# Kernel tuning notes

Measured on AMD Instinct MI355X. Metric: run time of the kernel, lower is better.

The kernel has to match this reference:

```python
import jax, jax.numpy as jnp
import numpy as np

N = 100_000           # nodes
E = 3_200_000         # edges (avg degree 32)
DIMS = [64, 80, 160, 112, 160, 176, 96, 144, 96, 128, 96, 160]
NUM_CLASSES = 2


def setup_inputs() -> dict:
    key = jax.random.key(0)
    ks = jax.random.split(key, 64)
    inp = {}
    inp['x'] = jax.random.normal(ks[0], (N, DIMS[0]), dtype=jnp.float32)
    inp['src'] = jax.random.randint(ks[1], (E,), 0, N, dtype=jnp.int32)
    inp['dst'] = jax.random.randint(ks[2], (E,), 0, N, dtype=jnp.int32)
    inp['edata'] = jax.random.uniform(ks[3], (E,), dtype=jnp.float32)
    for i in range(11):
        fi, fo = DIMS[i], DIMS[i + 1]
        inp[f'W{i+1}'] = jax.random.normal(ks[4 + i], (fi, fo), dtype=jnp.float32) / np.float32(np.sqrt(fi))
        inp[f'b{i+1}'] = jnp.zeros((fo,), dtype=jnp.float32)
    inp['Wd1'] = jax.random.normal(ks[20], (160, 140), dtype=jnp.float32) / np.float32(np.sqrt(160))
    inp['bd1'] = jnp.zeros((140,), dtype=jnp.float32)
    inp['Wd2'] = jax.random.normal(ks[21], (140, NUM_CLASSES), dtype=jnp.float32) / np.float32(np.sqrt(140))
    inp['bd2'] = jnp.zeros((NUM_CLASSES,), dtype=jnp.float32)
    inp['mu'] = jnp.asarray(0.0, dtype=jnp.float32)
    inp['sigma'] = jnp.asarray(1.0, dtype=jnp.float32)
    return inp


def _forward(x, src, dst, edata, Ws, bs, Wd1, bd1, Wd2, bd2, mu, sigma):
    n = x.shape[0]
    # edge-weight transform: keep w=1 edges, else gaussian kernel; mu/sigma read via .item() -> stop_gradient
    mu_c = jax.lax.stop_gradient(mu)
    sg_c = jax.lax.stop_gradient(sigma)
    w = jnp.where(edata == 1.0, edata, jnp.exp(-((edata - mu_c) ** 2) / sg_c))  # [E]
    ones_e = jnp.ones_like(edata)
    deg_out = jax.ops.segment_sum(ones_e, src, num_segments=n)  # [N]
    deg_in = jax.ops.segment_sum(ones_e, dst, num_segments=n)   # [N]
    ns = jnp.where(deg_out > 0, jax.lax.rsqrt(jnp.maximum(deg_out, 1.0)), 0.0)
    nd = jnp.where(deg_in > 0, jax.lax.rsqrt(jnp.maximum(deg_in, 1.0)), 0.0)
    coef = ns[src] * w  # [E] src-side norm fused with edge weight

    h = x
    for W, b in zip(Ws, bs):
        m = h[src] * coef[:, None]                               # gather + weight  [E, F]
        agg = jax.ops.segment_sum(m, dst, num_segments=n)        # scatter-add      [N, F]
        h = jax.nn.leaky_relu((agg * nd[:, None]) @ W + b)       # norm + linear + act

    h = jax.nn.leaky_relu(jnp.mean(h, axis=0))                   # mean_nodes -> [160]
    h = jax.nn.leaky_relu(h @ Wd1 + bd1)                         # dropout = identity (eval)
    return jax.nn.sigmoid(h @ Wd2 + bd2)                         # [NUM_CLASSES]


def reference(x, src, dst, edata,
              W1, b1, W2, b2, W3, b3, W4, b4, W5, b5, W6, b6,
              W7, b7, W8, b8, W9, b9, W10, b10, W11, b11,
              Wd1, bd1, Wd2, bd2, mu, sigma):
    Ws = [W1, W2, W3, W4, W5, W6, W7, W8, W9, W10, W11]
    bs = [b1, b2, b3, b4, b5, b6, b7, b8, b9, b10, b11]
    return _forward(x, src, dst, edata, Ws, bs, Wd1, bd1, Wd2, bd2, mu, sigma)
```

## Files before the change

### kernel.cpp

```cpp
#include <hip/hip_runtime.h>

#define LEAKY(v) ((v) > 0.0f ? (v) : 0.01f * (v))
#define SCAN_BLK 1024
#define EPB 4096
#define BKN 256

typedef __bf16 bf16x8 __attribute__((ext_vector_type(8)));
typedef float f32x4 __attribute__((ext_vector_type(4)));

__device__ inline float bflo(unsigned int u) { return __uint_as_float(u << 16); }
__device__ inline float bfhi(unsigned int u) { return __uint_as_float(u & 0xFFFF0000u); }
__device__ inline unsigned int pack2bf(float lo, float hi) {
    unsigned int a = __float_as_uint(lo);
    unsigned int b = __float_as_uint(hi);
    a = (a + 0x7FFFu + ((a >> 16) & 1u)) >> 16;
    b = (b + 0x7FFFu + ((b >> 16) & 1u)) & 0xFFFF0000u;
    return a | b;
}
__device__ inline unsigned short f2bf(float f) {
    unsigned int u = __float_as_uint(f);
    return (unsigned short)((u + 0x7FFFu + ((u >> 16) & 1u)) >> 16);
}

__device__ inline unsigned char f2f8(float v) {
    return (unsigned char)(__builtin_amdgcn_cvt_pk_fp8_f32(v, 0.0f, 0u, false) & 0xFFu);
}
__device__ inline uint2 pack8f8(float v0, float v1, float v2, float v3,
                                float v4, float v5, float v6, float v7) {
    uint2 q;
    q.x = __builtin_amdgcn_cvt_pk_fp8_f32(v0, v1, 0u, false);
    q.x = __builtin_amdgcn_cvt_pk_fp8_f32(v2, v3, q.x, true);
    q.y = __builtin_amdgcn_cvt_pk_fp8_f32(v4, v5, 0u, false);
    q.y = __builtin_amdgcn_cvt_pk_fp8_f32(v6, v7, q.y, true);
    return q;
}


__global__ void histo_kernel(const int* __restrict__ src, const int* __restrict__ dst,
                             int* __restrict__ bh_src, int* __restrict__ bh_dst,
                             int E, int NBK, int NBLK) {
    extern __shared__ int lds[];
    int* hs = lds;
    int* hd = lds + NBK;
    for (int j = threadIdx.x; j < 2 * NBK; j += 256) lds[j] = 0;
    __syncthreads();
    int b = blockIdx.x;
    int e0 = b * EPB, e1 = min(e0 + EPB, E);
    for (int e = e0 + threadIdx.x; e < e1; e += 256) {
        atomicAdd(&hs[src[e] >> 8], 1);
        atomicAdd(&hd[dst[e] >> 8], 1);
    }
    __syncthreads();
    for (int j = threadIdx.x; j < NBK; j += 256) {
        bh_src[j * NBLK + b] = hs[j];
        bh_dst[j * NBLK + b] = hd[j];
    }
}

__global__ void scan1_kernel(const int* __restrict__ deg, int* __restrict__ out,
                             int* __restrict__ bsums, int n) {
    __shared__ int sh[SCAN_BLK];
    int gid = blockIdx.x * SCAN_BLK + threadIdx.x;
    int v = (gid < n) ? deg[gid] : 0;
    sh[threadIdx.x] = v;
    __syncthreads();
    for (int off = 1; off < SCAN_BLK; off <<= 1) {
        int t = (threadIdx.x >= off) ? sh[threadIdx.x - off] : 0;
        __syncthreads();
        sh[threadIdx.x] += t;
        __syncthreads();
    }
    if (gid < n) out[gid + 1] = sh[threadIdx.x];
    if (threadIdx.x == SCAN_BLK - 1) bsums[blockIdx.x] = sh[threadIdx.x];
    if (gid == 0) out[0] = 0;
}

__global__ void scan2_kernel(int* __restrict__ bsums, int nb) {
    __shared__ int sh[SCAN_BLK];
    int v = (threadIdx.x < nb) ? bsums[threadIdx.x] : 0;
    sh[threadIdx.x] = v;
    __syncthreads();
    for (int off = 1; off < SCAN_BLK; off <<= 1) {
        int t = (threadIdx.x >= off) ? sh[threadIdx.x - off] : 0;
        __syncthreads();
        sh[threadIdx.x] += t;
        __syncthreads();
    }
    if (threadIdx.x < nb) bsums[threadIdx.x] = sh[threadIdx.x] - v;
}

__global__ void scan3_kernel(int* __restrict__ out, const int* __restrict__ bsums, int n) {
    int gid = blockIdx.x * SCAN_BLK + threadIdx.x;
    if (gid < n) out[gid + 1] += bsums[blockIdx.x];
}

__global__ void scat_src_kernel(const int* __restrict__ src, const int* __restrict__ bhs_src,
                                int* __restrict__ srcb, int E, int NBK, int NBLK) {
    extern __shared__ int cur[];
    int b = blockIdx.x;
    for (int j = threadIdx.x; j < NBK; j += 256) cur[j] = bhs_src[j * NBLK + b];
    __syncthreads();
    int e0 = b * EPB, e1 = min(e0 + EPB, E);
    for (int e = e0 + threadIdx.x; e < e1; e += 256) {
        int s = src[e];
        int pos = atomicAdd(&cur[s >> 8], 1);
        srcb[pos] = s;
    }
}

__global__ void ns_kernel(const int* __restrict__ srcb, const int* __restrict__ bhs_src,
                          float* __restrict__ ns, int n, int NBLK) {
    __shared__ int cnt[BKN];
    int b = blockIdx.x;
    int j = threadIdx.x;
    cnt[j] = 0;
    __syncthreads();
    int base = bhs_src[b * NBLK];
    int endp = bhs_src[(b + 1) * NBLK];
    for (int e = base + j; e < endp; e += 256)
        atomicAdd(&cnt[srcb[e] & 255], 1);
    __syncthreads();
    int node = b * BKN + j;
    if (node < n) {
        int c = cnt[j];
        ns[node] = (c > 0) ? rsqrtf((float)c) : 0.0f;
    }
}

__global__ void scat_dst_kernel(const int* __restrict__ src, const int* __restrict__ dst,
                                const float* __restrict__ edata, const float* __restrict__ ns,
                                const float* __restrict__ mu, const float* __restrict__ sigma,
                                const int* __restrict__ bhs_dst, int2* __restrict__ pay,
                                float* __restrict__ payw, int E, int NBK, int NBLK) {
    extern __shared__ int cur[];
    int b = blockIdx.x;
    for (int j = threadIdx.x; j < NBK; j += 256) cur[j] = bhs_dst[j * NBLK + b];
    __syncthreads();
    int e0 = b * EPB, e1 = min(e0 + EPB, E);
    for (int e = e0 + threadIdx.x; e < e1; e += 256) {
        int d = dst[e];
        int s = src[e];
        float ed = edata[e];
        float dd = ed - mu[0];
        float w = (ed == 1.0f) ? ed : expf(-(dd * dd) / sigma[0]);
        int pos = atomicAdd(&cur[d >> 8], 1);
        pay[pos] = make_int2(d, s);
        payw[pos] = ns[s] * w;
    }
}

__global__ void csr_kernel(const int2* __restrict__ pay, const float* __restrict__ payw,
                           const int* __restrict__ bhs_dst, int* __restrict__ rowptr,
                           float* __restrict__ nd, int2* __restrict__ es,
                           int n, int E, int NBK, int NBLK) {
    __shared__ int cnt[BKN];
    __shared__ int cur[BKN];
    int b = blockIdx.x;
    int j = threadIdx.x;
    cnt[j] = 0;
    __syncthreads();
    int base = bhs_dst[b * NBLK];
    int endp = bhs_dst[(b + 1) * NBLK];
    for (int e = base + j; e < endp; e += 256)
        atomicAdd(&cnt[pay[e].x & 255], 1);
    __syncthreads();
    int c0 = cnt[j];
    for (int off = 1; off < 256; off <<= 1) {
        int t = (j >= off) ? cnt[j - off] : 0;
        __syncthreads();
        cnt[j] += t;
        __syncthreads();
    }
    int excl = cnt[j] - c0;
    cur[j] = base + excl;
    int node = b * BKN + j;
    if (node < n) {
        rowptr[node] = base + excl;
        nd[node] = (c0 > 0) ? rsqrtf((float)c0) : 0.0f;
    }
    if (b == NBK - 1 && j == 0) rowptr[n] = E;
    __syncthreads();
    for (int e = base + j; e < endp; e += 256) {
        int2 p = pay[e];
        int pos = atomicAdd(&cur[p.x & 255], 1);
        es[pos] = make_int2(p.y, __float_as_int(payw[e]));
    }
}


__global__ void x2bf_kernel(const float* __restrict__ x, unsigned short* __restrict__ o16,
                            unsigned char* __restrict__ o8, long long total4) {
    long long i = (long long)blockIdx.x * blockDim.x + threadIdx.x;
    if (i < total4) {
        float4 v = *reinterpret_cast<const float4*>(&x[i * 4]);
        uint2 p;
        p.x = pack2bf(v.x, v.y);
        p.y = pack2bf(v.z, v.w);
        *reinterpret_cast<uint2*>(&o16[i * 4]) = p;
        unsigned int q = __builtin_amdgcn_cvt_pk_fp8_f32(v.x, v.y, 0u, false);
        q = __builtin_amdgcn_cvt_pk_fp8_f32(v.z, v.w, q, true);
        *reinterpret_cast<unsigned int*>(&o8[i * 4]) = q;
    }
}

__global__ void packW_kernel(const float* __restrict__ W, unsigned short* __restrict__ Wp,
                             int FI, int FO) {
    int KB = (FI + 31) / 32;
    int NB = FO / 16;
    int gid = blockIdx.x * blockDim.x + threadIdx.x;
    if (gid >= KB * NB * 64) return;
    int l = gid & 63;
    int tile = gid >> 6;
    int kb = tile % KB;
    int nb = tile / KB;
    int n = nb * 16 + (l & 15);
    int k0 = kb * 32 + (l >> 4) * 8;
    unsigned short tmp[8];
    #pragma unroll
    for (int j = 0; j < 8; ++j) {
        int k = k0 + j;
        tmp[j] = (k < FI) ? f2bf(W[(size_t)k * FO + n]) : (unsigned short)0;
    }
    *reinterpret_cast<uint4*>(&Wp[(size_t)gid * 8]) = *reinterpret_cast<uint4*>(tmp);
}

#define F8ACC(v, cc) { \
    auto p01 = __builtin_amdgcn_cvt_pk_f32_fp8((v).x, false); \
    auto p23 = __builtin_amdgcn_cvt_pk_f32_fp8((v).x, true);  \
    auto p45 = __builtin_amdgcn_cvt_pk_f32_fp8((v).y, false); \
    auto p67 = __builtin_amdgcn_cvt_pk_f32_fp8((v).y, true);  \
    a0 = fmaf(p01[0], cc, a0); a1 = fmaf(p01[1], cc, a1); \
    a2 = fmaf(p23[0], cc, a2); a3 = fmaf(p23[1], cc, a3); \
    a4 = fmaf(p45[0], cc, a4); a5 = fmaf(p45[1], cc, a5); \
    a6 = fmaf(p67[0], cc, a6); a7 = fmaf(p67[1], cc, a7); }

template<int MODE>
__global__ void agg_kernel(const unsigned char* __restrict__ h8,
                           const int* __restrict__ rowptr, const int2* __restrict__ es,
                           const float* __restrict__ nd, const float* __restrict__ bias,
                           unsigned short* __restrict__ out16, unsigned char* __restrict__ out8,
                           int n, int jt, int ng) {
    int g = threadIdx.x / jt;
    if (g >= ng) return;
    int i = blockIdx.x * ng + g;
    if (i >= n) return;
    int c = (threadIdx.x - g * jt) << 3;
    int F = jt << 3;
    int beg = rowptr[i], end = rowptr[i + 1];
    float a0 = 0, a1 = 0, a2 = 0, a3 = 0, a4 = 0, a5 = 0, a6 = 0, a7 = 0;
    int e = beg;
    for (; e + 4 <= end; e += 4) {
        int2 e0 = es[e + 0], e1 = es[e + 1], e2 = es[e + 2], e3 = es[e + 3];
        uint2 v0 = *reinterpret_cast<const uint2*>(&h8[(size_t)e0.x * F + c]);
        uint2 v1 = *reinterpret_cast<const uint2*>(&h8[(size_t)e1.x * F + c]);
        uint2 v2 = *reinterpret_cast<const uint2*>(&h8[(size_t)e2.x * F + c]);
        uint2 v3 = *reinterpret_cast<const uint2*>(&h8[(size_t)e3.x * F + c]);
        float c0 = __int_as_float(e0.y), c1 = __int_as_float(e1.y);
        float c2 = __int_as_float(e2.y), c3 = __int_as_float(e3.y);
        F8ACC(v0, c0)
        F8ACC(v1, c1)
        F8ACC(v2, c2)
        F8ACC(v3, c3)
    }
    for (; e < end; ++e) {
        int2 e0 = es[e];
        uint2 v0 = *reinterpret_cast<const uint2*>(&h8[(size_t)e0.x * F + c]);
        float c0 = __int_as_float(e0.y);
        F8ACC(v0, c0)
    }
    if (MODE) {
        float s = nd[i];
        a0 = a0 * s + bias[c + 0]; a0 = LEAKY(a0);
        a1 = a1 * s + bias[c + 1]; a1 = LEAKY(a1);
        a2 = a2 * s + bias[c + 2]; a2 = LEAKY(a2);
        a3 = a3 * s + bias[c + 3]; a3 = LEAKY(a3);
        a4 = a4 * s + bias[c + 4]; a4 = LEAKY(a4);
        a5 = a5 * s + bias[c + 5]; a5 = LEAKY(a5);
        a6 = a6 * s + bias[c + 6]; a6 = LEAKY(a6);
        a7 = a7 * s + bias[c + 7]; a7 = LEAKY(a7);
    }
    uint4 p;
    p.x = pack2bf(a0, a1); p.y = pack2bf(a2, a3);
    p.z = pack2bf(a4, a5); p.w = pack2bf(a6, a7);
    *reinterpret_cast<uint4*>(&out16[(size_t)i * F + c]) = p;
    if (MODE) {
        uint2 q = pack8f8(a0, a1, a2, a3, a4, a5, a6, a7);
        *reinterpret_cast<uint2*>(&out8[(size_t)i * F + c]) = q;
    }
}

template<int FI, int FO, int MODE>
__global__ __launch_bounds__(256) void mm_mfma_kernel(
    const unsigned short* __restrict__ Ab, const float* __restrict__ nd,
    const unsigned short* __restrict__ Wp, const float* __restrict__ bias,
    unsigned short* __restrict__ out16, unsigned char* __restrict__ out8, int n)
{
    constexpr int FIP = (FI + 31) / 32 * 32;
    constexpr int KB = FIP / 32;
    constexpr int NB = FO / 16;
    constexpr int LDA = FIP + 8;
    constexpr int RW = FIP / 8;
    __shared__ unsigned short As[64 * LDA];

    const int t = threadIdx.x;
    const int row0 = blockIdx.x * 64;

    for (int idx = t; idx < 64 * RW; idx += 256) {
        int r = idx / RW;
        int c8 = (idx - r * RW) * 8;
        int grow = row0 + r;
        uint4 v = make_uint4(0u, 0u, 0u, 0u);
        if (grow < n && c8 < FI)
            v = *reinterpret_cast<const uint4*>(&Ab[(size_t)grow * FI + c8]);
        *reinterpret_cast<uint4*>(&As[r * LDA + c8]) = v;
    }
    __syncthreads();

    const int w = t >> 6;
    const int l = t & 63;
    const int arow = (w << 4) + (l & 15);
    const int koff = (l >> 4) << 3;

    bf16x8 a[KB];
    #pragma unroll
    for (int kb = 0; kb < KB; ++kb)
        a[kb] = *reinterpret_cast<const bf16x8*>(&As[arow * LDA + kb * 32 + koff]);

    f32x4 acc[NB] = {};
    #pragma unroll
    for (int nb = 0; nb < NB; ++nb) {
        #pragma unroll
        for (int kb = 0; kb < KB; ++kb) {
            bf16x8 b = *reinterpret_cast<const bf16x8*>(&Wp[(size_t)((nb * KB + kb) * 64 + l) * 8]);
            acc[nb] = __builtin_amdgcn_mfma_f32_16x16x32_bf16(a[kb], b, acc[nb], 0, 0, 0);
        }
    }

    const int col = l & 15;
    const int rb = (l >> 4) << 2;
    #pragma unroll
    for (int r = 0; r < 4; ++r) {
        int grow = row0 + (w << 4) + rb + r;
        if (grow < n) {
            float s = MODE ? nd[grow] : 1.0f;
            #pragma unroll
            for (int nb = 0; nb < NB; ++nb) {
                float v = acc[nb][r];
                if (MODE) {
                    v = v * s + bias[nb * 16 + col];
                    v = LEAKY(v);
                    out16[(size_t)grow * FO + nb * 16 + col] = f2bf(v);
                    out8[(size_t)grow * FO + nb * 16 + col] = f2f8(v);
                } else {
                    out8[(size_t)grow * FO + nb * 16 + col] = f2f8(v);
                }
            }
        }
    }
}

__global__ void mean_kernel(const unsigned short* __restrict__ h, float* __restrict__ acc,
                            int n, int F) {
    int f = threadIdx.x;
    if (f >= F) return;
    float partial = 0.0f;
    for (int i = blockIdx.x; i < n; i += gridDim.x) {
        partial += __uint_as_float(((unsigned int)h[(size_t)i * F + f]) << 16);
    }
    atomicAdd(&acc[f], partial);
}

__global__ void head_kernel(const float* __restrict__ acc, const float* __restrict__ Wd1,
                            const float* __restrict__ bd1, const float* __restrict__ Wd2,
                            const float* __restrict__ bd2, float* __restrict__ out, int n) {
    __shared__ float gm[160];
    __shared__ float h1[140];
    int tid = threadIdx.x;
    if (tid < 160) {
        float v = acc[tid] / (float)n;
        gm[tid] = LEAKY(v);
    }
    __syncthreads();
    if (tid < 140) {
        float s = bd1[tid];
        for (int k = 0; k < 160; ++k) s += gm[k] * Wd1[k * 140 + tid];
        h1[tid] = LEAKY(s);
    }
    __syncthreads();
    if (tid < 2) {
        float s = bd2[tid];
        for (int k = 0; k < 140; ++k) s += h1[k] * Wd2[k * 2 + tid];
        out[tid] = 1.0f / (1.0f + expf(-s));
    }
}

extern "C" void kernel_launch(void* const* d_in, const int* in_sizes, int n_in,
                              void* d_out, int out_size, void* d_ws, size_t ws_size,
                              hipStream_t stream) {
    static const int dims[12] = {64, 80, 160, 112, 160, 176, 96, 144, 96, 128, 96, 160};

    const float* x     = (const float*)d_in[0];
    const int*   src   = (const int*)d_in[1];
    const int*   dst   = (const int*)d_in[2];
    const float* edata = (const float*)d_in[3];
    const float* W[11];
    const float* B[11];
    for (int i = 0; i < 11; ++i) {
        W[i] = (const float*)d_in[4 + 2 * i];
        B[i] = (const float*)d_in[5 + 2 * i];
    }
    const float* Wd1   = (const float*)d_in[26];
    const float* bd1   = (const float*)d_in[27];
    const float* Wd2   = (const float*)d_in[28];
    const float* bd2   = (const float*)d_in[29];
    const float* mu    = (const float*)d_in[30];
    const float* sigma = (const float*)d_in[31];
    float* out = (float*)d_out;

    const int N = in_sizes[0] / 64;
    const int E = in_sizes[1];
    const int FMAX = 176;

    const int NBK  = (N + BKN - 1) / BKN;
    const int NBLK = (E + EPB - 1) / EPB;
    const int LEN  = NBK * NBLK;

    size_t woff[11];
    size_t wtot = 0;
    for (int l = 0; l < 11; ++l) {
        woff[l] = wtot;
        int fip = (dims[l] + 31) / 32 * 32;
        wtot += (size_t)fip * dims[l + 1];
    }

    char* wsb = (char*)d_ws;
    size_t o = 0;
    auto alloc = [&](size_t bytes) { void* p = wsb + o; o += (bytes + 255) & ~(size_t)255; return p; };
    unsigned short* hb_main = (unsigned short*)alloc((size_t)N * FMAX * 2);
    unsigned short* hb_t    = (unsigned short*)alloc((size_t)N * FMAX * 2);
    unsigned char*  h8_main = (unsigned char*) alloc((size_t)N * FMAX);
    unsigned char*  h8_t    = (unsigned char*) alloc((size_t)N * FMAX);
    unsigned short* Wp  = (unsigned short*)alloc(wtot * 2);
    int2*  es      = (int2*) alloc((size_t)E * sizeof(int2));
    int2*  pay     = (int2*) alloc((size_t)E * sizeof(int2));
    float* payw    = (float*)alloc((size_t)E * sizeof(float));
    int*   srcb    = (int*)  alloc((size_t)E * sizeof(int));
    int*   bh_src  = (int*)  alloc((size_t)LEN * sizeof(int));
    int*   bhs_src = (int*)  alloc((size_t)(LEN + 1) * sizeof(int));
    int*   bh_dst  = (int*)  alloc((size_t)LEN * sizeof(int));
    int*   bhs_dst = (int*)  alloc((size_t)(LEN + 1) * sizeof(int));
    int*   rowptr  = (int*)  alloc((size_t)(N + 1) * sizeof(int));
    float* ns      = (float*)alloc((size_t)N * sizeof(float));
    float* nd      = (float*)alloc((size_t)N * sizeof(float));
    int*   bsums   = (int*)  alloc(2048 * sizeof(int));
    float* acc     = (float*)alloc(160 * sizeof(float));

    histo_kernel<<<NBLK, 256, 2 * NBK * sizeof(int), stream>>>(src, dst, bh_src, bh_dst,
                                                               E, NBK, NBLK);
    int snb = (LEN + SCAN_BLK - 1) / SCAN_BLK;
    scan1_kernel<<<snb, SCAN_BLK, 0, stream>>>(bh_src, bhs_src, bsums, LEN);
    scan2_kernel<<<1, SCAN_BLK, 0, stream>>>(bsums, snb);
    scan3_kernel<<<snb, SCAN_BLK, 0, stream>>>(bhs_src, bsums, LEN);
    scan1_kernel<<<snb, SCAN_BLK, 0, stream>>>(bh_dst, bhs_dst, bsums, LEN);
    scan2_kernel<<<1, SCAN_BLK, 0, stream>>>(bsums, snb);
    scan3_kernel<<<snb, SCAN_BLK, 0, stream>>>(bhs_dst, bsums, LEN);
    scat_src_kernel<<<NBLK, 256, NBK * sizeof(int), stream>>>(src, bhs_src, srcb, E, NBK, NBLK);
    ns_kernel<<<NBK, 256, 0, stream>>>(srcb, bhs_src, ns, N, NBLK);
    scat_dst_kernel<<<NBLK, 256, NBK * sizeof(int), stream>>>(src, dst, edata, ns, mu, sigma,
                                                              bhs_dst, pay, payw, E, NBK, NBLK);
    csr_kernel<<<NBK, 256, 0, stream>>>(pay, payw, bhs_dst, rowptr, nd, es, N, E, NBK, NBLK);

    long long x4 = (long long)N * 64 / 4;
    x2bf_kernel<<<(int)((x4 + 255) / 256), 256, 0, stream>>>(x, hb_main, h8_main, x4);
    for (int l = 0; l < 11; ++l) {
        int fip = (dims[l] + 31) / 32 * 32;
        int threads = (fip / 32) * (dims[l + 1] / 16) * 64;
        packW_kernel<<<(threads + 255) / 256, 256, 0, stream>>>(W[l], Wp + woff[l],
                                                                dims[l], dims[l + 1]);
    }

    const int mmgrid = (N + 63) / 64;

    #define DO_A(FI, FO, l) { \
        constexpr int jt = FI / 8; constexpr int ng = 256 / jt; \
        agg_kernel<0><<<(N + ng - 1) / ng, 256, 0, stream>>>( \
            h8_main, rowptr, es, nd, B[l], hb_t, nullptr, N, jt, ng); \
        mm_mfma_kernel<FI, FO, 1><<<mmgrid, 256, 0, stream>>>( \
            hb_t, nd, Wp + woff[l], B[l], hb_main, h8_main, N); }

    #define DO_B(FI, FO, l) { \
        mm_mfma_kernel<FI, FO, 0><<<mmgrid, 256, 0, stream>>>( \
            hb_main, nd, Wp + woff[l], B[l], nullptr, h8_t, N); \
        constexpr int jt = FO / 8; constexpr int ng = 256 / jt; \
        agg_kernel<1><<<(N + ng - 1) / ng, 256, 0, stream>>>( \
            h8_t, rowptr, es, nd, B[l], hb_main, h8_main, N, jt, ng); }

    DO_A(64, 80, 0)
    DO_A(80, 160, 1)
    DO_B(160, 112, 2)
    DO_A(112, 160, 3)
    DO_A(160, 176, 4)
    DO_B(176, 96, 5)
    DO_A(96, 144, 6)
    DO_B(144, 96, 7)
    DO_A(96, 128, 8)
    DO_B(128, 96, 9)
    DO_A(96, 160, 10)

    #undef DO_A
    #undef DO_B

    hipMemsetAsync(acc, 0, 160 * sizeof(float), stream);
    mean_kernel<<<256, 160, 0, stream>>>(hb_main, acc, N, 160);
    head_kernel<<<1, 256, 0, stream>>>(acc, Wd1, bd1, Wd2, bd2, out, N);
}
```

Before: 1.379 ms.

## Fuse src/dst bucket scatter, merge histogram scans, compact payloads, unroll aggregation by 8

Concatenates the src and dst bucket histograms so a single three-kernel scan covers both, and fuses the two scatter passes into one kernel with 512 threads. The payload is compacted: only the low 8 bits of each src id are stored for the degree count, and the dst low byte is packed into the top byte of the src id. The ns multiplication moves into the CSR build, so scatter no longer depends on ns. The aggregation inner loop is unrolled to eight edges to expose more memory-level parallelism, at the cost of more registers. Packing src into 24 bits assumes fewer than 16M nodes.

New measurement: 1.349 ms. -2.2%, faster.

```diff
diff --git a/kernel.cpp b/kernel.cpp
--- a/kernel.cpp
+++ b/kernel.cpp
@@ -37,23 +37,22 @@
 
 
 __global__ void histo_kernel(const int* __restrict__ src, const int* __restrict__ dst,
-                             int* __restrict__ bh_src, int* __restrict__ bh_dst,
-                             int E, int NBK, int NBLK) {
+                             int* __restrict__ bh, int E, int NBK, int NBLK, int LEN) {
     extern __shared__ int lds[];
     int* hs = lds;
     int* hd = lds + NBK;
-    for (int j = threadIdx.x; j < 2 * NBK; j += 256) lds[j] = 0;
+    for (int j = threadIdx.x; j < 2 * NBK; j += 512) lds[j] = 0;
     __syncthreads();
     int b = blockIdx.x;
     int e0 = b * EPB, e1 = min(e0 + EPB, E);
-    for (int e = e0 + threadIdx.x; e < e1; e += 256) {
+    for (int e = e0 + threadIdx.x; e < e1; e += 512) {
         atomicAdd(&hs[src[e] >> 8], 1);
         atomicAdd(&hd[dst[e] >> 8], 1);
     }
     __syncthreads();
-    for (int j = threadIdx.x; j < NBK; j += 256) {
-        bh_src[j * NBLK + b] = hs[j];
-        bh_dst[j * NBLK + b] = hd[j];
+    for (int j = threadIdx.x; j < NBK; j += 512) {
+        bh[j * NBLK + b] = hs[j];
+        bh[LEN + j * NBLK + b] = hd[j];
     }
 }
 
@@ -94,31 +93,45 @@
     if (gid < n) out[gid + 1] += bsums[blockIdx.x];
 }
 
-__global__ void scat_src_kernel(const int* __restrict__ src, const int* __restrict__ bhs_src,
-                                int* __restrict__ srcb, int E, int NBK, int NBLK) {
+__global__ void scat_kernel(const int* __restrict__ src, const int* __restrict__ dst,
+                            const float* __restrict__ edata,
+                            const float* __restrict__ mu, const float* __restrict__ sigma,
+                            const int* __restrict__ bhs, unsigned char* __restrict__ srcb8,
+                            int2* __restrict__ pay, int E, int NBK, int NBLK, int LEN) {
     extern __shared__ int cur[];
+    int* cs = cur;
+    int* cd = cur + NBK;
     int b = blockIdx.x;
-    for (int j = threadIdx.x; j < NBK; j += 256) cur[j] = bhs_src[j * NBLK + b];
+    for (int j = threadIdx.x; j < NBK; j += 512) {
+        cs[j] = bhs[j * NBLK + b];
+        cd[j] = bhs[LEN + j * NBLK + b] - E;
+    }
     __syncthreads();
     int e0 = b * EPB, e1 = min(e0 + EPB, E);
-    for (int e = e0 + threadIdx.x; e < e1; e += 256) {
+    for (int e = e0 + threadIdx.x; e < e1; e += 512) {
         int s = src[e];
-        int pos = atomicAdd(&cur[s >> 8], 1);
-        srcb[pos] = s;
-    }
-}
-
-__global__ void ns_kernel(const int* __restrict__ srcb, const int* __restrict__ bhs_src,
+        int d = dst[e];
+        float ed = edata[e];
+        float dd = ed - mu[0];
+        float w = (ed == 1.0f) ? ed : expf(-(dd * dd) / sigma[0]);
+        int ps = atomicAdd(&cs[s >> 8], 1);
+        srcb8[ps] = (unsigned char)(s & 255);
+        int pd = atomicAdd(&cd[d >> 8], 1);
+        pay[pd] = make_int2(s | ((d & 255) << 24), __float_as_int(w));
+    }
+}
+
+__global__ void ns_kernel(const unsigned char* __restrict__ srcb8, const int* __restrict__ bhs,
                           float* __restrict__ ns, int n, int NBLK) {
     __shared__ int cnt[BKN];
     int b = blockIdx.x;
     int j = threadIdx.x;
     cnt[j] = 0;
     __syncthreads();
-    int base = bhs_src[b * NBLK];
-    int endp = bhs_src[(b + 1) * NBLK];
+    int base = bhs[b * NBLK];
+    int endp = bhs[(b + 1) * NBLK];
     for (int e = base + j; e < endp; e += 256)
-        atomicAdd(&cnt[srcb[e] & 255], 1);
+        atomicAdd(&cnt[srcb8[e]], 1);
     __syncthreads();
     int node = b * BKN + j;
     if (node < n) {
@@ -127,42 +140,20 @@
     }
 }
 
-__global__ void scat_dst_kernel(const int* __restrict__ src, const int* __restrict__ dst,
-                                const float* __restrict__ edata, const float* __restrict__ ns,
-                                const float* __restrict__ mu, const float* __restrict__ sigma,
-                                const int* __restrict__ bhs_dst, int2* __restrict__ pay,
-                                float* __restrict__ payw, int E, int NBK, int NBLK) {
-    extern __shared__ int cur[];
-    int b = blockIdx.x;
-    for (int j = threadIdx.x; j < NBK; j += 256) cur[j] = bhs_dst[j * NBLK + b];
-    __syncthreads();
-    int e0 = b * EPB, e1 = min(e0 + EPB, E);
-    for (int e = e0 + threadIdx.x; e < e1; e += 256) {
-        int d = dst[e];
-        int s = src[e];
-        float ed = edata[e];
-        float dd = ed - mu[0];
-        float w = (ed == 1.0f) ? ed : expf(-(dd * dd) / sigma[0]);
-        int pos = atomicAdd(&cur[d >> 8], 1);
-        pay[pos] = make_int2(d, s);
-        payw[pos] = ns[s] * w;
-    }
-}
-
-__global__ void csr_kernel(const int2* __restrict__ pay, const float* __restrict__ payw,
-                           const int* __restrict__ bhs_dst, int* __restrict__ rowptr,
+__global__ void csr_kernel(const int2* __restrict__ pay, const float* __restrict__ ns,
+                           const int* __restrict__ bhs, int* __restrict__ rowptr,
                            float* __restrict__ nd, int2* __restrict__ es,
-                           int n, int E, int NBK, int NBLK) {
+                           int n, int E, int NBK, int NBLK, int LEN) {
     __shared__ int cnt[BKN];
     __shared__ int cur[BKN];
     int b = blockIdx.x;
     int j = threadIdx.x;
     cnt[j] = 0;
     __syncthreads();
-    int base = bhs_dst[b * NBLK];
-    int endp = bhs_dst[(b + 1) * NBLK];
+    int base = bhs[LEN + b * NBLK] - E;
+    int endp = bhs[LEN + (b + 1) * NBLK] - E;
     for (int e = base + j; e < endp; e += 256)
-        atomicAdd(&cnt[pay[e].x & 255], 1);
+        atomicAdd(&cnt[(pay[e].x >> 24) & 255], 1);
     __syncthreads();
     int c0 = cnt[j];
     for (int off = 1; off < 256; off <<= 1) {
@@ -182,8 +173,10 @@
     __syncthreads();
     for (int e = base + j; e < endp; e += 256) {
         int2 p = pay[e];
-        int pos = atomicAdd(&cur[p.x & 255], 1);
-        es[pos] = make_int2(p.y, __float_as_int(payw[e]));
+        int s = p.x & 0x00FFFFFF;
+        float coef = ns[s] * __int_as_float(p.y);
+        int pos = atomicAdd(&cur[(p.x >> 24) & 255], 1);
+        es[pos] = make_int2(s, __float_as_int(coef));
     }
 }
 
@@ -249,18 +242,19 @@
     int beg = rowptr[i], end = rowptr[i + 1];
     float a0 = 0, a1 = 0, a2 = 0, a3 = 0, a4 = 0, a5 = 0, a6 = 0, a7 = 0;
     int e = beg;
-    for (; e + 4 <= end; e += 4) {
-        int2 e0 = es[e + 0], e1 = es[e + 1], e2 = es[e + 2], e3 = es[e + 3];
-        uint2 v0 = *reinterpret_cast<const uint2*>(&h8[(size_t)e0.x * F + c]);
-        uint2 v1 = *reinterpret_cast<const uint2*>(&h8[(size_t)e1.x * F + c]);
-        uint2 v2 = *reinterpret_cast<const uint2*>(&h8[(size_t)e2.x * F + c]);
-        uint2 v3 = *reinterpret_cast<const uint2*>(&h8[(size_t)e3.x * F + c]);
-        float c0 = __int_as_float(e0.y), c1 = __int_as_float(e1.y);
-        float c2 = __int_as_float(e2.y), c3 = __int_as_float(e3.y);
-        F8ACC(v0, c0)
-        F8ACC(v1, c1)
-        F8ACC(v2, c2)
-        F8ACC(v3, c3)
+    for (; e + 8 <= end; e += 8) {
+        int2 ee[8];
+        uint2 vv[8];
+        #pragma unroll
+        for (int q = 0; q < 8; ++q) ee[q] = es[e + q];
+        #pragma unroll
+        for (int q = 0; q < 8; ++q)
+            vv[q] = *reinterpret_cast<const uint2*>(&h8[(size_t)ee[q].x * F + c]);
+        #pragma unroll
+        for (int q = 0; q < 8; ++q) {
+            float cc = __int_as_float(ee[q].y);
+            F8ACC(vv[q], cc)
+        }
     }
     for (; e < end; ++e) {
         int2 e0 = es[e];
@@ -443,32 +437,24 @@
     unsigned short* Wp  = (unsigned short*)alloc(wtot * 2);
     int2*  es      = (int2*) alloc((size_t)E * sizeof(int2));
     int2*  pay     = (int2*) alloc((size_t)E * sizeof(int2));
-    float* payw    = (float*)alloc((size_t)E * sizeof(float));
-    int*   srcb    = (int*)  alloc((size_t)E * sizeof(int));
-    int*   bh_src  = (int*)  alloc((size_t)LEN * sizeof(int));
-    int*   bhs_src = (int*)  alloc((size_t)(LEN + 1) * sizeof(int));
-    int*   bh_dst  = (int*)  alloc((size_t)LEN * sizeof(int));
-    int*   bhs_dst = (int*)  alloc((size_t)(LEN + 1) * sizeof(int));
+    unsigned char* srcb8 = (unsigned char*)alloc((size_t)E);
+    int*   bh      = (int*)  alloc((size_t)(2 * LEN) * sizeof(int));
+    int*   bhs     = (int*)  alloc((size_t)(2 * LEN + 1) * sizeof(int));
     int*   rowptr  = (int*)  alloc((size_t)(N + 1) * sizeof(int));
     float* ns      = (float*)alloc((size_t)N * sizeof(float));
     float* nd      = (float*)alloc((size_t)N * sizeof(float));
     int*   bsums   = (int*)  alloc(2048 * sizeof(int));
     float* acc     = (float*)alloc(160 * sizeof(float));
 
-    histo_kernel<<<NBLK, 256, 2 * NBK * sizeof(int), stream>>>(src, dst, bh_src, bh_dst,
-                                                               E, NBK, NBLK);
-    int snb = (LEN + SCAN_BLK - 1) / SCAN_BLK;
-    scan1_kernel<<<snb, SCAN_BLK, 0, stream>>>(bh_src, bhs_src, bsums, LEN);
+    histo_kernel<<<NBLK, 512, 2 * NBK * sizeof(int), stream>>>(src, dst, bh, E, NBK, NBLK, LEN);
+    int snb = (2 * LEN + SCAN_BLK - 1) / SCAN_BLK;
+    scan1_kernel<<<snb, SCAN_BLK, 0, stream>>>(bh, bhs, bsums, 2 * LEN);
     scan2_kernel<<<1, SCAN_BLK, 0, stream>>>(bsums, snb);
-    scan3_kernel<<<snb, SCAN_BLK, 0, stream>>>(bhs_src, bsums, LEN);
-    scan1_kernel<<<snb, SCAN_BLK, 0, stream>>>(bh_dst, bhs_dst, bsums, LEN);
-    scan2_kernel<<<1, SCAN_BLK, 0, stream>>>(bsums, snb);
-    scan3_kernel<<<snb, SCAN_BLK, 0, stream>>>(bhs_dst, bsums, LEN);
-    scat_src_kernel<<<NBLK, 256, NBK * sizeof(int), stream>>>(src, bhs_src, srcb, E, NBK, NBLK);
-    ns_kernel<<<NBK, 256, 0, stream>>>(srcb, bhs_src, ns, N, NBLK);
-    scat_dst_kernel<<<NBLK, 256, NBK * sizeof(int), stream>>>(src, dst, edata, ns, mu, sigma,
-                                                              bhs_dst, pay, payw, E, NBK, NBLK);
-    csr_kernel<<<NBK, 256, 0, stream>>>(pay, payw, bhs_dst, rowptr, nd, es, N, E, NBK, NBLK);
+    scan3_kernel<<<snb, SCAN_BLK, 0, stream>>>(bhs, bsums, 2 * LEN);
+    scat_kernel<<<NBLK, 512, 2 * NBK * sizeof(int), stream>>>(src, dst, edata, mu, sigma,
+                                                              bhs, srcb8, pay, E, NBK, NBLK, LEN);
+    ns_kernel<<<NBK, 256, 0, stream>>>(srcb8, bhs, ns, N, NBLK);
+    csr_kernel<<<NBK, 256, 0, stream>>>(pay, ns, bhs, rowptr, nd, es, N, E, NBK, NBLK, LEN);
 
     long long x4 = (long long)N * 64 / 4;
     x2bf_kernel<<<(int)((x4 + 255) / 256), 256, 0, stream>>>(x, hb_main, h8_main, x4);
```
